# Kernel tuning notes

Measured on AMD Instinct MI355X. Metric: run time of the kernel, lower is better.

Reference implementation:

```python
import jax, jax.numpy as jnp
from jax import lax
import numpy as np

B, K, H, W = 16, 8, 256, 256


def setup_inputs() -> dict:
    key = jax.random.key(0)
    masks = jax.random.normal(key, (B, K, H, W), dtype=jnp.float32)
    return {"masks": masks}


def _nlccs_loss_one(mask):
    """Per-mask loss. mask: (H, W) float, already rescaled/clamped.

    Replicates cv2.connectedComponentsWithStats (8-connectivity, background is
    a single label regardless of connectivity), sorts components by area, and
    suppresses (zeroes a pmask over) the bounding box of the second-largest
    component, then returns mean(pmask * mask).
    """
    h, w = mask.shape
    S = h * w  # sentinel / background label
    sent = jnp.int32(S)
    fg = lax.stop_gradient(mask) > 0.5  # cv2 threshold (arr > 0.5)
    idx = jnp.arange(S, dtype=jnp.int32).reshape(h, w)
    lab0 = jnp.where(fg, idx, sent)

    def step(lab):
        # 8-connectivity neighbor-min propagation (cv2 default connectivity=8)
        p = jnp.pad(lab, 1, constant_values=S)
        m = lab
        for dy in (-1, 0, 1):
            for dx in (-1, 0, 1):
                if dy == 0 and dx == 0:
                    continue
                m = jnp.minimum(m, p[1 + dy:1 + dy + h, 1 + dx:1 + dx + w])
        lab = jnp.where(fg, m, sent)
        # pointer jumping: lab <- lab[lab] for log-time convergence
        ext = jnp.concatenate([lab.reshape(-1), jnp.array([S], jnp.int32)])
        return jnp.where(fg, ext[lab], sent)

    def cond(c):
        lab, prev = c
        return jnp.any(lab != prev)

    def body(c):
        lab, _ = c
        return step(lab), lab

    lab, _ = lax.while_loop(cond, body, (step(lab0), lab0))

    # per-label areas; background pixels all share label S (like cv2 label 0)
    areas = jnp.zeros(S + 1, jnp.int32).at[lab.reshape(-1)].add(1)
    _, top_idx = lax.top_k(areas, 2)
    second = top_idx[1]  # stats sorted by area -> stats[-2]

    # bounding box of the second-largest component
    sel = lab == second
    rows = jnp.arange(h, dtype=jnp.int32)[:, None]
    cols = jnp.arange(w, dtype=jnp.int32)[None, :]
    h0 = jnp.min(jnp.where(sel, rows, h))
    h1 = jnp.max(jnp.where(sel, rows, -1)) + 1
    w0 = jnp.min(jnp.where(sel, cols, w))
    w1 = jnp.max(jnp.where(sel, cols, -1)) + 1
    inside = (rows >= h0) & (rows < h1) & (cols >= w0) & (cols < w1)
    pmask = 1.0 - inside.astype(mask.dtype)  # pmask[h0:h1, w0:w1] = 0
    return (pmask * mask).mean()


def reference(masks):
    # masks: (b, k, h, w)
    m = jnp.maximum((masks + 1.0) * 0.5, 0.0)  # ((masks+1)/2).clamp(min=0)
    flat = m.reshape(-1, m.shape[-2], m.shape[-1])  # (b*k, h, w)
    losses = jax.vmap(_nlccs_loss_one)(flat)
    return losses.mean()
```

## Files before the change

kernel.cpp:

```cpp
#include <hip/hip_runtime.h>

#define HH 256
#define WW 256
#define SS 65536
#define NM 128
#define TRR 16
#define NT2 16
#define RMX 2048
#define SPT 1024
#define SPM 16384

struct Meta {
  double dsum[NM];
  int h0[NM]; int h1[NM]; int w0[NM]; int w1[NM];
};

__device__ __forceinline__ int find_c(int* L, int x) {
  int p = L[x];
  if (p == x) return x;
  int root = p, q = L[root];
  while (q != root) { root = q; q = L[root]; }
  if (root != p) L[x] = root;
  return root;
}

__device__ void unite(int* L, int a, int b) {
  bool done = false;
  do {
    a = find_c(L, a);
    b = find_c(L, b);
    if (a < b)      { int old = atomicMin(&L[b], a); done = (old == b); b = old; }
    else if (b < a) { int old = atomicMin(&L[a], b); done = (old == a); a = old; }
    else done = true;
  } while (!done);
}

__device__ __forceinline__ int find_halve(int* L, int x) {
  int p = L[x];
  while (p != x) {
    int gp = L[p];
    if (gp == p) return p;
    L[x] = gp;
    x = p; p = gp;
  }
  return x;
}

__device__ __forceinline__ int cid(const unsigned long long* rm,
                                   const int* rpre, int r) {
  int w = r >> 6, b = r & 63;
  return rpre[w] + (int)__popcll(rm[w] & (b ? ((1ull << b) - 1) : 0ull));
}

__device__ __forceinline__ unsigned long long mask_le(int b) {
  return (b == 63) ? ~0ull : ((1ull << (b + 1)) - 1);
}
__device__ __forceinline__ unsigned long long mask_lt(int b) {
  return b ? ((1ull << b) - 1) : 0ull;
}

__global__ __launch_bounds__(512)
void k_local(const float* __restrict__ in, int cb,
             int* __restrict__ gp, int* __restrict__ ga,
             unsigned int* __restrict__ gbb, unsigned short* __restrict__ gl,
             unsigned short* __restrict__ gbrow, int* __restrict__ gnr,
             double* __restrict__ tdsum, unsigned int* __restrict__ tbb,
             int* __restrict__ gfg0) {
  __shared__ unsigned long long sfgw[TRR][4];
  __shared__ unsigned char sfgc[TRR][32];
  __shared__ unsigned long long srs[TRR][4];
  __shared__ int wpre64[64];
  __shared__ int snr;
  __shared__ int sspan[RMX];
  __shared__ int suf[RMX];
  __shared__ unsigned long long rootm[32];
  __shared__ int rpre[32];
  __shared__ int sA[SPT], sW0[SPT], sW1[SPT], sH0[SPT], sH1[SPT];
  __shared__ double sred[8];
  __shared__ int sbb[4][8];

  int q = blockIdx.x, lm = q >> 4, tile = q & 15;
  int tid = threadIdx.x, lane = tid & 63, wv = tid >> 6;
  int gm = cb + lm, R0 = tile << 4;

  int r1 = tid >> 5, cs = tid & 31;
  const float4* src =
      (const float4*)(in + ((size_t)gm << 16) + ((R0 + r1) << 8) + (cs << 3));
  double dsum = 0.0;
  unsigned int fgb = 0;
  for (int k = 0; k < 2; k++) {
    float4 v = src[k];
    float m0 = fmaxf((v.x + 1.0f) * 0.5f, 0.0f);
    float m1 = fmaxf((v.y + 1.0f) * 0.5f, 0.0f);
    float m2 = fmaxf((v.z + 1.0f) * 0.5f, 0.0f);
    float m3 = fmaxf((v.w + 1.0f) * 0.5f, 0.0f);
    dsum += (double)m0 + (double)m1 + (double)m2 + (double)m3;
    fgb |= ((m0 > 0.5f) ? 1u : 0u) << (4 * k);
    fgb |= ((m1 > 0.5f) ? 1u : 0u) << (4 * k + 1);
    fgb |= ((m2 > 0.5f) ? 1u : 0u) << (4 * k + 2);
    fgb |= ((m3 > 0.5f) ? 1u : 0u) << (4 * k + 3);
  }
  sfgc[r1][cs] = (unsigned char)fgb;
  __syncthreads();
  if (tid < 64) {
    int row = tid >> 2, w = tid & 3;
    const unsigned char* pc = &sfgc[row][w << 3];
    unsigned long long wd = 0;
    for (int i = 0; i < 8; i++) wd |= ((unsigned long long)pc[i]) << (i << 3);
    sfgw[row][w] = wd;
  }
  __syncthreads();

  if (tid < 64) {
    int row = tid >> 2, w = tid & 3;
    unsigned long long W = sfgw[row][w];
    unsigned long long carry = (w > 0) ? (sfgw[row][w - 1] >> 63) : 0ull;
    unsigned long long rs = W & ~((W << 1) | carry);
    srs[row][w] = rs;
    int cnt = (int)__popcll(rs);
    int sa = cnt;
    for (int off = 1; off < 64; off <<= 1) {
      int t = __shfl_up(sa, off);
      if (tid >= off) sa += t;
    }
    wpre64[tid] = sa - cnt;
    if (tid == 63) snr = sa;
    int id = sa - cnt;
    unsigned long long bits = rs;
    while (bits) {
      int a = (int)__ffsll(bits) - 1;
      bits &= bits - 1;
      int A = (w << 6) + a;
      unsigned long long inv = ~(W >> a);
      int len = inv ? ((int)__ffsll(inv) - 1) : (64 - a);
      if (len == 64 - a) {
        for (int w2 = w + 1; w2 < 4; w2++) {
          unsigned long long iv2 = ~sfgw[row][w2];
          int t = iv2 ? ((int)__ffsll(iv2) - 1) : 64;
          len += t;
          if (t < 64) break;
        }
      }
      sspan[id] = (row << 16) | (A << 8) | (A + len - 1);
      suf[id] = id;
      id++;
    }
  } else {
    for (int s = tid - 64; s < SPT; s += 448) {
      sA[s] = 0; sW0[s] = WW; sW1[s] = -1; sH0[s] = TRR; sH1[s] = -1;
    }
  }
  __syncthreads();

  int nr = snr;

  for (int i = tid; i < nr; i += 512) {
    int sp = sspan[i];
    int row = sp >> 16, a = (sp >> 8) & 255, b = sp & 255;
    if (row == 0) continue;
    int lo = max(a - 1, 0), hi = min(b + 1, 255);
    const unsigned long long* Wp = sfgw[row - 1];
    const unsigned long long* Rp = srs[row - 1];
    int prebase = (row - 1) << 2;
    int lw = lo >> 6, lb = lo & 63;
    if (((Wp[lw] >> lb) & 1) && !((Rp[lw] >> lb) & 1)) {
      int j = wpre64[prebase + lw] + (int)__popcll(Rp[lw] & mask_le(lb)) - 1;
      unite(suf, i, j);
    }
    for (int w = lw; w <= (hi >> 6); w++) {
      unsigned long long m = Rp[w];
      if (w == lw) m &= ~mask_lt(lb);
      if (w == (hi >> 6)) m &= mask_le(hi & 63);
      int base2 = wpre64[prebase + w];
      while (m) {
        int bb = (int)__ffsll(m) - 1;
        m &= m - 1;
        int j = base2 + (int)__popcll(Rp[w] & mask_lt(bb));
        unite(suf, i, j);
      }
    }
  }
  __syncthreads();

  for (int j = 0; j < 4; j++) {
    int i = tid + (j << 9);
    unsigned long long bal = __ballot(i < nr && suf[i] == i);
    if (lane == 0) rootm[wv + (j << 3)] = bal;
  }
  __syncthreads();
  if (tid < 32) {
    int pc = (int)__popcll(rootm[tid]);
    int sa = pc;
    for (int off = 1; off < 32; off <<= 1) {
      int t = __shfl_up(sa, off);
      if (tid >= off) sa += t;
    }
    rpre[tid] = sa - pc;
  }
  __syncthreads();

  for (int i = tid; i < nr; i += 512) {
    int root = find_halve(suf, i);
    int id = cid(rootm, rpre, root);
    int sp = sspan[i];
    int row = sp >> 16, a = (sp >> 8) & 255, b = sp & 255;
    atomicAdd(&sA[id], b - a + 1);
    if (a < sW0[id]) atomicMin(&sW0[id], a);
    if (b > sW1[id]) atomicMax(&sW1[id], b);
    if (row < sH0[id]) atomicMin(&sH0[id], row);
    if (row > sH1[id]) atomicMax(&sH1[id], row);
  }
  __syncthreads();

  int nc = rpre[31] + (int)__popcll(rootm[31]);
  for (int i = tid; i < nr; i += 512) {
    if (suf[i] == i) {
      int id = cid(rootm, rpre, i);
      int gid = (lm << 14) + (tile << 10) + id;
      int sp = sspan[i];
      gp[gid] = gid;
      ga[gid] = sA[id];
      gl[gid] = (unsigned short)((tile << 12) + ((sp >> 16) << 8) +
                                 ((sp >> 8) & 255));
      gbb[gid] = ((unsigned)(R0 + sH0[id]) << 24) | ((unsigned)sW0[id] << 16)
               | ((unsigned)(R0 + sH1[id]) << 8) | (unsigned)sW1[id];
    }
  }
  {
    int c = tid & 255, topbot = tid >> 8;
    int brow = topbot ? (TRR - 1) : 0;
    unsigned short val = 0xFFFF;
    if ((sfgw[brow][c >> 6] >> (c & 63)) & 1) {
      int w = c >> 6, bb = c & 63;
      int id = wpre64[(brow << 2) + w] +
               (int)__popcll(srs[brow][w] & mask_le(bb)) - 1;
      int root = find_halve(suf, id);
      val = (unsigned short)((tile << 10) + cid(rootm, rpre, root));
    }
    gbrow[(q << 9) + (topbot ? 256 : 0) + c] = val;
  }
  if (tid == 0) gnr[q] = nc;

  int c = tid & 255, half = (tid >> 8) << 3;
  int bh0r = TRR, bh1r = -1;
  bool anybg = false;
  for (int row = half; row < half + 8; row++) {
    if (!((sfgw[row][c >> 6] >> (c & 63)) & 1)) {
      anybg = true;
      bh0r = min(bh0r, row); bh1r = max(bh1r, row);
    }
  }
  int bw0r = anybg ? c : WW, bw1r = anybg ? c : -1;
  for (int off = 32; off > 0; off >>= 1) {
    bw0r = min(bw0r, __shfl_down(bw0r, off));
    bw1r = max(bw1r, __shfl_down(bw1r, off));
    bh0r = min(bh0r, __shfl_down(bh0r, off));
    bh1r = max(bh1r, __shfl_down(bh1r, off));
  }
  if (lane == 0) { sbb[0][wv] = bw0r; sbb[1][wv] = bw1r;
                   sbb[2][wv] = bh0r; sbb[3][wv] = bh1r; }
  for (int off = 32; off > 0; off >>= 1) dsum += __shfl_down(dsum, off);
  if (lane == 0) sred[wv] = dsum;
  __syncthreads();
  if (tid == 0) {
    int a0 = sbb[0][0], a1 = sbb[1][0], a2 = sbb[2][0], a3 = sbb[3][0];
    for (int i = 1; i < 8; i++) {
      a0 = min(a0, sbb[0][i]); a1 = max(a1, sbb[1][i]);
      a2 = min(a2, sbb[2][i]); a3 = max(a3, sbb[3][i]);
    }
    unsigned pack = (a1 >= 0)
        ? (((unsigned)(R0 + a2) << 24) | ((unsigned)a0 << 16) |
           ((unsigned)(R0 + a3) << 8) | (unsigned)a1)
        : 0xFFFF0000u;
    tbb[q] = pack;
    double t = 0.0;
    for (int i = 0; i < 8; i++) t += sred[i];
    tdsum[q] = t;
    if (tile == 0) gfg0[lm] = (int)(sfgw[0][0] & 1ull);
  }
}

__global__ void k_seam(int* __restrict__ gp,
                       const unsigned short* __restrict__ gbrow) {
  int b = blockIdx.x;
  int lm = b / 15, s = b % 15;
  int tb = lm << 4;
  int sbase = lm << 14;
  const unsigned short* up = gbrow + ((tb + s) << 9) + 256;
  const unsigned short* lo = gbrow + ((tb + s + 1) << 9);
  int c = threadIdx.x;
  unsigned short v16 = lo[c];
  if (v16 == 0xFFFF) return;
  int v = sbase + v16;
  bool wfg = (c > 0) && (lo[c - 1] != 0xFFFF);
  unsigned short n16 = up[c];
  if (!wfg) {
    if (n16 != 0xFFFF) unite(gp, v, sbase + n16);
    else if (c > 0 && up[c - 1] != 0xFFFF) unite(gp, v, sbase + up[c - 1]);
  }
  if (n16 == 0xFFFF && c < 255 && up[c + 1] != 0xFFFF)
    unite(gp, v, sbase + up[c + 1]);
}

__global__ void k_push(int* __restrict__ gp, int* __restrict__ ga,
                       unsigned int* __restrict__ gbb,
                       const int* __restrict__ gnr) {
  int q = blockIdx.x;
  int lm = q >> 4;
  int sbase = lm << 14;
  int nc = gnr[q];
  int tid = threadIdx.x, lane = tid & 63;
  for (int t = 0; t < 4; t++) {
    int slot = (t << 8) + tid;
    int r = -1, a = 0;
    int h0 = HH, w0 = WW, h1 = -1, w1 = -1;
    if (slot < nc) {
      int gid = sbase + ((q & 15) << 10) + slot;
      int rr = find_c(gp, gid);
      if (rr != gid) {
        r = rr; a = ga[gid];
        unsigned int bb = gbb[gid];
        h0 = (int)(bb >> 24); w0 = (int)((bb >> 16) & 255);
        h1 = (int)((bb >> 8) & 255); w1 = (int)(bb & 255);
      }
    }
    bool pend = (r >= 0);
    while (__any(pend)) {
      unsigned long long mk = __ballot(pend);
      int srcl = (int)__ffsll(mk) - 1;
      int lead = __shfl(r, srcl);
      bool mine = pend && (r == lead);
      int v  = mine ? a  : 0;
      int g0 = mine ? h0 : HH;
      int g1 = mine ? h1 : -1;
      int g2 = mine ? w0 : WW;
      int g3 = mine ? w1 : -1;
      for (int off = 32; off > 0; off >>= 1) {
        v += __shfl_down(v, off);
        g0 = min(g0, __shfl_down(g0, off));
        g1 = max(g1, __shfl_down(g1, off));
        g2 = min(g2, __shfl_down(g2, off));
        g3 = max(g3, __shfl_down(g3, off));
      }
      int tot = __shfl(v, 0);
      int m0 = __shfl(g0, 0), m1 = __shfl(g1, 0);
      int m2 = __shfl(g2, 0), m3 = __shfl(g3, 0);
      if (lane == srcl) {
        atomicAdd(&ga[lead], tot);
        unsigned int* dst = &gbb[lead];
        unsigned int old = *dst;
        while (true) {
          int oh0 = (int)(old >> 24), ow0 = (int)((old >> 16) & 255);
          int oh1 = (int)((old >> 8) & 255), ow1 = (int)(old & 255);
          int nh0 = min(oh0, m0), nw0 = min(ow0, m2);
          int nh1 = max(oh1, m1), nw1 = max(ow1, m3);
          unsigned int mrg = ((unsigned)nh0 << 24) | ((unsigned)nw0 << 16) |
                             ((unsigned)nh1 << 8) | (unsigned)nw1;
          if (mrg == old) break;
          unsigned int got = atomicCAS(dst, old, mrg);
          if (got == old) break;
          old = got;
        }
      }
      pend = pend && !mine;
    }
  }
}

__global__ void k_top2p(const int* __restrict__ gp, const int* __restrict__ ga,
                        const unsigned short* __restrict__ gl,
                        const int* __restrict__ gnr,
                        unsigned long long* __restrict__ tt1,
                        unsigned long long* __restrict__ tt2,
                        int* __restrict__ tfs) {
  int q = blockIdx.x;
  int lm = q >> 4, tile = q & 15;
  int sbase = lm << 14;
  int nc = gnr[q];
  int tid = threadIdx.x, lane = tid & 63, wv = tid >> 6;
  unsigned long long t1 = 0, t2 = 0;
  int fsum = 0;
  for (int sl = tid; sl < nc; sl += 256) {
    int s = (tile << 10) + sl;
    int gid = sbase + s;
    if (gp[gid] == gid) {
      int a = ga[gid];
      int lab = gl[gid];
      fsum += a;
      unsigned long long key = ((unsigned long long)a << 37)
                             | ((unsigned long long)(SS - lab) << 20)
                             | (unsigned)s;
      if (key > t1) { t2 = t1; t1 = key; }
      else if (key > t2) t2 = key;
    }
  }
  for (int off = 32; off > 0; off >>= 1) {
    unsigned long long o1 = __shfl_down(t1, off), o2 = __shfl_down(t2, off);
    if (o1 > t1) { t2 = (t1 > o2) ? t1 : o2; t1 = o1; }
    else if (o1 > t2) t2 = o1;
    fsum += __shfl_down(fsum, off);
  }
  __shared__ unsigned long long s1[4], s2[4];
  __shared__ int sf[4];
  if (lane == 0) { s1[wv] = t1; s2[wv] = t2; sf[wv] = fsum; }
  __syncthreads();
  if (tid == 0) {
    for (int i = 1; i < 4; i++) {
      unsigned long long o1 = s1[i], o2 = s2[i];
      if (o1 > t1) { t2 = (t1 > o2) ? t1 : o2; t1 = o1; }
      else if (o1 > t2) t2 = o1;
      fsum += sf[i];
    }
    tt1[q] = t1; tt2[q] = t2; tfs[q] = fsum;
  }
}

__global__ __launch_bounds__(64)
void k_mask(const double* __restrict__ tdsum,
            const unsigned int* __restrict__ tbb,
            const unsigned long long* __restrict__ tt1,
            const unsigned long long* __restrict__ tt2,
            const int* __restrict__ tfs, const int* __restrict__ gfg0,
            const unsigned int* __restrict__ gbb,
            Meta* __restrict__ mt, int c0) {
  int lm = blockIdx.x, gm = c0 + lm;
  int tid = threadIdx.x;
  int tb = lm << 4;
  double d = 0.0;
  int h0 = 255, w0 = 255, h1 = 0, w1 = 0;
  unsigned long long t1 = 0, t2 = 0;
  int fsum = 0;
  if (tid < 16) {
    d = tdsum[tb + tid];
    unsigned bb = tbb[tb + tid];
    h0 = (int)(bb >> 24); w0 = (int)((bb >> 16) & 255);
    h1 = (int)((bb >> 8) & 255); w1 = (int)(bb & 255);
    t1 = tt1[tb + tid]; t2 = tt2[tb + tid]; fsum = tfs[tb + tid];
  }
  for (int off = 8; off > 0; off >>= 1) {
    d += __shfl_down(d, off);
    h0 = min(h0, __shfl_down(h0, off));
    w0 = min(w0, __shfl_down(w0, off));
    h1 = max(h1, __shfl_down(h1, off));
    w1 = max(w1, __shfl_down(w1, off));
    unsigned long long o1 = __shfl_down(t1, off), o2 = __shfl_down(t2, off);
    if (o1 > t1) { t2 = (t1 > o2) ? t1 : o2; t1 = o1; }
    else if (o1 > t2) t2 = o1;
    fsum += __shfl_down(fsum, off);
  }
  if (tid == 0) {
    mt->dsum[gm] = d;
    unsigned long long bg = ((unsigned long long)(SS - fsum)) << 37;
    int zl = gfg0[lm] ? 1 : 0;
    unsigned long long zk = ((unsigned long long)(SS - zl)) << 20;
    if (bg > t1) { t2 = t1; t1 = bg; } else if (bg > t2) t2 = bg;
    if (zk > t1) { t2 = t1; t1 = zk; } else if (zk > t2) t2 = zk;
    if (t2 == bg) {
      mt->h0[gm] = h0; mt->h1[gm] = h1; mt->w0[gm] = w0; mt->w1[gm] = w1;
    } else if (t2 == zk) {
      mt->h0[gm] = 1; mt->h1[gm] = 0; mt->w0[gm] = 1; mt->w1[gm] = 0;
    } else {
      unsigned int bb = gbb[(lm << 14) + (int)(t2 & 0xFFFFF)];
      mt->h0[gm] = (int)(bb >> 24);
      mt->w0[gm] = (int)((bb >> 16) & 255);
      mt->h1[gm] = (int)((bb >> 8) & 255);
      mt->w1[gm] = (int)(bb & 255);
    }
  }
}

__global__ void k_inside(const float* __restrict__ in,
                         const Meta* __restrict__ mt,
                         double* __restrict__ dinsp, int c0) {
  int b = blockIdx.x;
  int lm = b >> 3, seg = b & 7;
  int gm = c0 + lm;
  int h0 = mt->h0[gm], h1 = mt->h1[gm], w0 = mt->w0[gm], w1 = mt->w1[gm];
  double acc = 0.0;
  if (h1 >= h0) {
    int cc = w0 + threadIdx.x;
    if (cc <= w1) {
      const float* base = in + ((size_t)gm << 16);
      for (int rr = h0 + seg; rr <= h1; rr += 8) {
        float x = base[(rr << 8) + cc];
        acc += (double)fmaxf((x + 1.0f) * 0.5f, 0.0f);
      }
    }
  }
  for (int off = 32; off > 0; off >>= 1) acc += __shfl_down(acc, off);
  __shared__ double sd[4];
  int wid = threadIdx.x >> 6, lane = threadIdx.x & 63;
  if (lane == 0) sd[wid] = acc;
  __syncthreads();
  if (threadIdx.x == 0)
    dinsp[(gm << 3) + seg] = sd[0] + sd[1] + sd[2] + sd[3];
}

__global__ void k_final(const Meta* __restrict__ mt,
                        const double* __restrict__ dinsp,
                        float* __restrict__ out) {
  __shared__ double sd[NM];
  int t = threadIdx.x;
  double di = 0.0;
  for (int s = 0; s < 8; s++) di += dinsp[(t << 3) + s];
  sd[t] = (mt->dsum[t] - di) / (double)SS;
  __syncthreads();
  for (int off = 64; off > 0; off >>= 1) {
    if (t < off) sd[t] += sd[t + off];
    __syncthreads();
  }
  if (t == 0) out[0] = (float)(sd[0] / (double)NM);
}

extern "C" void kernel_launch(void* const* d_in, const int* in_sizes, int n_in,
                              void* d_out, int out_size, void* d_ws,
                              size_t ws_size, hipStream_t stream) {
  const float* in = (const float*)d_in[0];
  float* out = (float*)d_out;

  Meta* mt = (Meta*)d_ws;
  const size_t meta_bytes = (sizeof(Meta) + 255) & ~(size_t)255;
  char* base = (char*)d_ws + meta_bytes;
  size_t fixed = (size_t)NM * 8 * sizeof(double);
  size_t avail = (ws_size > meta_bytes + fixed)
                     ? (ws_size - meta_bytes - fixed) : 0;
  const size_t per_mask = (size_t)NT2 * 8 + NT2 * 4 + 4 +
                          (size_t)SPM * (4 + 4 + 4 + 2) +
                          (size_t)NT2 * 512 * 2 + NT2 * 4 +
                          (size_t)NT2 * (8 + 8 + 4);
  int chunk = (int)(avail / per_mask);
  if (chunk > NM) chunk = NM;
  if (chunk < 1) return;

  char* ptr = base;
  double* dinsp = (double*)ptr;        ptr += fixed;
  double* tdsum = (double*)ptr;        ptr += (size_t)chunk * NT2 * 8;
  unsigned long long* tt1 = (unsigned long long*)ptr;
  ptr += (size_t)chunk * NT2 * 8;
  unsigned long long* tt2 = (unsigned long long*)ptr;
  ptr += (size_t)chunk * NT2 * 8;
  int* gp = (int*)ptr;                 ptr += (size_t)chunk * SPM * 4;
  int* ga = (int*)ptr;                 ptr += (size_t)chunk * SPM * 4;
  unsigned int* gbb = (unsigned int*)ptr;       ptr += (size_t)chunk * SPM * 4;
  unsigned short* gl = (unsigned short*)ptr;    ptr += (size_t)chunk * SPM * 2;
  unsigned short* gbrow = (unsigned short*)ptr; ptr += (size_t)chunk * NT2 * 512 * 2;
  int* gnr = (int*)ptr;                ptr += (size_t)chunk * NT2 * 4;
  unsigned int* tbb = (unsigned int*)ptr;       ptr += (size_t)chunk * NT2 * 4;
  int* tfs = (int*)ptr;                ptr += (size_t)chunk * NT2 * 4;
  int* gfg0 = (int*)ptr;

  for (int c0 = 0; c0 < NM; c0 += chunk) {
    int cn = (chunk < NM - c0) ? chunk : (NM - c0);
    k_local<<<cn * NT2, 512, 0, stream>>>(in, c0, gp, ga, gbb, gl, gbrow,
                                          gnr, tdsum, tbb, gfg0);
    k_seam <<<cn * 15, 256, 0, stream>>>(gp, gbrow);
    k_push <<<cn * NT2, 256, 0, stream>>>(gp, ga, gbb, gnr);
    k_top2p<<<cn * NT2, 256, 0, stream>>>(gp, ga, gl, gnr, tt1, tt2, tfs);
    k_mask <<<cn, 64, 0, stream>>>(tdsum, tbb, tt1, tt2, tfs, gfg0, gbb,
                                   mt, c0);
    k_inside<<<cn * 8, 256, 0, stream>>>(in, mt, dinsp, c0);
  }
  k_final<<<1, 128, 0, stream>>>(mt, dinsp, out);
}
```

Before: 184.6 us.

## Fold seam, mask and final kernels into predecessors via last-block counters

Removes three separate kernel launches per chunk (seam union, per-mask metadata, final reduction) by appending their work to the preceding kernels. Each preceding kernel's last-finishing block does the extra work, found with an atomic counter plus threadfence. The counters are zeroed by one memset each call. This cuts launch and inter-kernel gaps, at the cost of serialising the seam unions inside a single block per mask and adding atomic and fence overhead.

```diff
diff --git a/kernel.cpp b/kernel.cpp
--- a/kernel.cpp
+++ b/kernel.cpp
@@ -65,7 +65,7 @@
              unsigned int* __restrict__ gbb, unsigned short* __restrict__ gl,
              unsigned short* __restrict__ gbrow, int* __restrict__ gnr,
              double* __restrict__ tdsum, unsigned int* __restrict__ tbb,
-             int* __restrict__ gfg0) {
+             int* __restrict__ gfg0, int* __restrict__ cntA) {
   __shared__ unsigned long long sfgw[TRR][4];
   __shared__ unsigned char sfgc[TRR][32];
   __shared__ unsigned long long srs[TRR][4];
@@ -78,6 +78,7 @@
   __shared__ int sA[SPT], sW0[SPT], sW1[SPT], sH0[SPT], sH1[SPT];
   __shared__ double sred[8];
   __shared__ int sbb[4][8];
+  __shared__ int slast;
 
   int q = blockIdx.x, lm = q >> 4, tile = q & 15;
   int tid = threadIdx.x, lane = tid & 63, wv = tid >> 6;
@@ -278,28 +279,32 @@
     tdsum[q] = t;
     if (tile == 0) gfg0[lm] = (int)(sfgw[0][0] & 1ull);
   }
-}
-
-__global__ void k_seam(int* __restrict__ gp,
-                       const unsigned short* __restrict__ gbrow) {
-  int b = blockIdx.x;
-  int lm = b / 15, s = b % 15;
-  int tb = lm << 4;
-  int sbase = lm << 14;
-  const unsigned short* up = gbrow + ((tb + s) << 9) + 256;
-  const unsigned short* lo = gbrow + ((tb + s + 1) << 9);
-  int c = threadIdx.x;
-  unsigned short v16 = lo[c];
-  if (v16 == 0xFFFF) return;
-  int v = sbase + v16;
-  bool wfg = (c > 0) && (lo[c - 1] != 0xFFFF);
-  unsigned short n16 = up[c];
-  if (!wfg) {
-    if (n16 != 0xFFFF) unite(gp, v, sbase + n16);
-    else if (c > 0 && up[c - 1] != 0xFFFF) unite(gp, v, sbase + up[c - 1]);
-  }
-  if (n16 == 0xFFFF && c < 255 && up[c + 1] != 0xFFFF)
-    unite(gp, v, sbase + up[c + 1]);
+
+  __threadfence();
+  __syncthreads();
+  if (tid == 0) slast = (atomicAdd(&cntA[gm], 1) == 15) ? 1 : 0;
+  __syncthreads();
+  if (slast) {
+    __threadfence();
+    int sbase = lm << 14;
+    for (int idx = tid; idx < 15 * 256; idx += 512) {
+      int s = idx >> 8, c2 = idx & 255;
+      const unsigned short* up = gbrow + (((lm << 4) + s) << 9) + 256;
+      const unsigned short* lo = gbrow + (((lm << 4) + s + 1) << 9);
+      unsigned short v16 = lo[c2];
+      if (v16 == 0xFFFF) continue;
+      int v = sbase + v16;
+      bool wfg = (c2 > 0) && (lo[c2 - 1] != 0xFFFF);
+      unsigned short n16 = up[c2];
+      if (!wfg) {
+        if (n16 != 0xFFFF) unite(gp, v, sbase + n16);
+        else if (c2 > 0 && up[c2 - 1] != 0xFFFF)
+          unite(gp, v, sbase + up[c2 - 1]);
+      }
+      if (n16 == 0xFFFF && c2 < 255 && up[c2 + 1] != 0xFFFF)
+        unite(gp, v, sbase + up[c2 + 1]);
+    }
+  }
 }
 
 __global__ void k_push(int* __restrict__ gp, int* __restrict__ ga,
@@ -372,12 +377,20 @@
                         const int* __restrict__ gnr,
                         unsigned long long* __restrict__ tt1,
                         unsigned long long* __restrict__ tt2,
-                        int* __restrict__ tfs) {
+                        int* __restrict__ tfs,
+                        const double* __restrict__ tdsum,
+                        const unsigned int* __restrict__ tbb,
+                        const int* __restrict__ gfg0,
+                        const unsigned int* __restrict__ gbb,
+                        int* __restrict__ cntB,
+                        Meta* __restrict__ mt, int c0) {
   int q = blockIdx.x;
   int lm = q >> 4, tile = q & 15;
+  int gm = c0 + lm;
   int sbase = lm << 14;
   int nc = gnr[q];
   int tid = threadIdx.x, lane = tid & 63, wv = tid >> 6;
+  __shared__ int slast;
   unsigned long long t1 = 0, t2 = 0;
   int fsum = 0;
   for (int sl = tid; sl < nc; sl += 256) {
@@ -413,65 +426,63 @@
     }
     tt1[q] = t1; tt2[q] = t2; tfs[q] = fsum;
   }
-}
-
-__global__ __launch_bounds__(64)
-void k_mask(const double* __restrict__ tdsum,
-            const unsigned int* __restrict__ tbb,
-            const unsigned long long* __restrict__ tt1,
-            const unsigned long long* __restrict__ tt2,
-            const int* __restrict__ tfs, const int* __restrict__ gfg0,
-            const unsigned int* __restrict__ gbb,
-            Meta* __restrict__ mt, int c0) {
-  int lm = blockIdx.x, gm = c0 + lm;
-  int tid = threadIdx.x;
-  int tb = lm << 4;
-  double d = 0.0;
-  int h0 = 255, w0 = 255, h1 = 0, w1 = 0;
-  unsigned long long t1 = 0, t2 = 0;
-  int fsum = 0;
-  if (tid < 16) {
-    d = tdsum[tb + tid];
-    unsigned bb = tbb[tb + tid];
-    h0 = (int)(bb >> 24); w0 = (int)((bb >> 16) & 255);
-    h1 = (int)((bb >> 8) & 255); w1 = (int)(bb & 255);
-    t1 = tt1[tb + tid]; t2 = tt2[tb + tid]; fsum = tfs[tb + tid];
-  }
-  for (int off = 8; off > 0; off >>= 1) {
-    d += __shfl_down(d, off);
-    h0 = min(h0, __shfl_down(h0, off));
-    w0 = min(w0, __shfl_down(w0, off));
-    h1 = max(h1, __shfl_down(h1, off));
-    w1 = max(w1, __shfl_down(w1, off));
-    unsigned long long o1 = __shfl_down(t1, off), o2 = __shfl_down(t2, off);
-    if (o1 > t1) { t2 = (t1 > o2) ? t1 : o2; t1 = o1; }
-    else if (o1 > t2) t2 = o1;
-    fsum += __shfl_down(fsum, off);
-  }
-  if (tid == 0) {
-    mt->dsum[gm] = d;
-    unsigned long long bg = ((unsigned long long)(SS - fsum)) << 37;
-    int zl = gfg0[lm] ? 1 : 0;
-    unsigned long long zk = ((unsigned long long)(SS - zl)) << 20;
-    if (bg > t1) { t2 = t1; t1 = bg; } else if (bg > t2) t2 = bg;
-    if (zk > t1) { t2 = t1; t1 = zk; } else if (zk > t2) t2 = zk;
-    if (t2 == bg) {
-      mt->h0[gm] = h0; mt->h1[gm] = h1; mt->w0[gm] = w0; mt->w1[gm] = w1;
-    } else if (t2 == zk) {
-      mt->h0[gm] = 1; mt->h1[gm] = 0; mt->w0[gm] = 1; mt->w1[gm] = 0;
-    } else {
-      unsigned int bb = gbb[(lm << 14) + (int)(t2 & 0xFFFFF)];
-      mt->h0[gm] = (int)(bb >> 24);
-      mt->w0[gm] = (int)((bb >> 16) & 255);
-      mt->h1[gm] = (int)((bb >> 8) & 255);
-      mt->w1[gm] = (int)(bb & 255);
+
+  __threadfence();
+  __syncthreads();
+  if (tid == 0) slast = (atomicAdd(&cntB[gm], 1) == 15) ? 1 : 0;
+  __syncthreads();
+  if (slast && wv == 0) {
+    __threadfence();
+    int tb = lm << 4;
+    double d = 0.0;
+    int h0 = 255, w0 = 255, h1 = 0, w1 = 0;
+    unsigned long long u1 = 0, u2 = 0;
+    int fs = 0;
+    if (lane < 16) {
+      d = tdsum[tb + lane];
+      unsigned bb = tbb[tb + lane];
+      h0 = (int)(bb >> 24); w0 = (int)((bb >> 16) & 255);
+      h1 = (int)((bb >> 8) & 255); w1 = (int)(bb & 255);
+      u1 = tt1[tb + lane]; u2 = tt2[tb + lane]; fs = tfs[tb + lane];
+    }
+    for (int off = 8; off > 0; off >>= 1) {
+      d += __shfl_down(d, off);
+      h0 = min(h0, __shfl_down(h0, off));
+      w0 = min(w0, __shfl_down(w0, off));
+      h1 = max(h1, __shfl_down(h1, off));
+      w1 = max(w1, __shfl_down(w1, off));
+      unsigned long long o1 = __shfl_down(u1, off), o2 = __shfl_down(u2, off);
+      if (o1 > u1) { u2 = (u1 > o2) ? u1 : o2; u1 = o1; }
+      else if (o1 > u2) u2 = o1;
+      fs += __shfl_down(fs, off);
+    }
+    if (lane == 0) {
+      mt->dsum[gm] = d;
+      unsigned long long bg = ((unsigned long long)(SS - fs)) << 37;
+      int zl = gfg0[lm] ? 1 : 0;
+      unsigned long long zk = ((unsigned long long)(SS - zl)) << 20;
+      if (bg > u1) { u2 = u1; u1 = bg; } else if (bg > u2) u2 = bg;
+      if (zk > u1) { u2 = u1; u1 = zk; } else if (zk > u2) u2 = zk;
+      if (u2 == bg) {
+        mt->h0[gm] = h0; mt->h1[gm] = h1; mt->w0[gm] = w0; mt->w1[gm] = w1;
+      } else if (u2 == zk) {
+        mt->h0[gm] = 1; mt->h1[gm] = 0; mt->w0[gm] = 1; mt->w1[gm] = 0;
+      } else {
+        unsigned int bb = gbb[(lm << 14) + (int)(u2 & 0xFFFFF)];
+        mt->h0[gm] = (int)(bb >> 24);
+        mt->w0[gm] = (int)((bb >> 16) & 255);
+        mt->h1[gm] = (int)((bb >> 8) & 255);
+        mt->w1[gm] = (int)(bb & 255);
+      }
     }
   }
 }
 
 __global__ void k_inside(const float* __restrict__ in,
                          const Meta* __restrict__ mt,
-                         double* __restrict__ dinsp, int c0) {
+                         double* __restrict__ dinsp, int c0,
+                         int* __restrict__ cntC, int nb, int do_final,
+                         float* __restrict__ out) {
   int b = blockIdx.x;
   int lm = b >> 3, seg = b & 7;
   int gm = c0 + lm;
@@ -494,22 +505,31 @@
   __syncthreads();
   if (threadIdx.x == 0)
     dinsp[(gm << 3) + seg] = sd[0] + sd[1] + sd[2] + sd[3];
-}
-
-__global__ void k_final(const Meta* __restrict__ mt,
-                        const double* __restrict__ dinsp,
-                        float* __restrict__ out) {
-  __shared__ double sd[NM];
-  int t = threadIdx.x;
-  double di = 0.0;
-  for (int s = 0; s < 8; s++) di += dinsp[(t << 3) + s];
-  sd[t] = (mt->dsum[t] - di) / (double)SS;
-  __syncthreads();
-  for (int off = 64; off > 0; off >>= 1) {
-    if (t < off) sd[t] += sd[t + off];
+
+  if (do_final) {
+    __shared__ int sflag;
+    if (threadIdx.x == 0) {
+      __threadfence();
+      sflag = (atomicAdd(cntC, 1) == nb - 1) ? 1 : 0;
+    }
     __syncthreads();
-  }
-  if (t == 0) out[0] = (float)(sd[0] / (double)NM);
+    if (sflag) {
+      __threadfence();
+      __shared__ double sd2[NM];
+      int t = threadIdx.x;
+      if (t < NM) {
+        double di = 0.0;
+        for (int s = 0; s < 8; s++) di += dinsp[(t << 3) + s];
+        sd2[t] = (mt->dsum[t] - di) / (double)SS;
+      }
+      __syncthreads();
+      for (int off = 64; off > 0; off >>= 1) {
+        if (t < off) sd2[t] += sd2[t + off];
+        __syncthreads();
+      }
+      if (t == 0) out[0] = (float)(sd2[0] / (double)NM);
+    }
+  }
 }
 
 extern "C" void kernel_launch(void* const* d_in, const int* in_sizes, int n_in,
@@ -521,7 +541,8 @@
   Meta* mt = (Meta*)d_ws;
   const size_t meta_bytes = (sizeof(Meta) + 255) & ~(size_t)255;
   char* base = (char*)d_ws + meta_bytes;
-  size_t fixed = (size_t)NM * 8 * sizeof(double);
+  const size_t cnt_bytes = ((size_t)(NM * 2 + 1) * 4 + 255) & ~(size_t)255;
+  size_t fixed = (size_t)NM * 8 * sizeof(double) + cnt_bytes;
   size_t avail = (ws_size > meta_bytes + fixed)
                      ? (ws_size - meta_bytes - fixed) : 0;
   const size_t per_mask = (size_t)NT2 * 8 + NT2 * 4 + 4 +
@@ -533,7 +554,11 @@
   if (chunk < 1) return;
 
   char* ptr = base;
-  double* dinsp = (double*)ptr;        ptr += fixed;
+  double* dinsp = (double*)ptr;        ptr += (size_t)NM * 8 * 8;
+  int* cntA = (int*)ptr;
+  int* cntB = cntA + NM;
+  int* cntC = cntB + NM;
+  ptr += cnt_bytes;
   double* tdsum = (double*)ptr;        ptr += (size_t)chunk * NT2 * 8;
   unsigned long long* tt1 = (unsigned long long*)ptr;
   ptr += (size_t)chunk * NT2 * 8;
@@ -549,16 +574,18 @@
   int* tfs = (int*)ptr;                ptr += (size_t)chunk * NT2 * 4;
   int* gfg0 = (int*)ptr;
 
+  hipMemsetAsync(cntA, 0, (size_t)(NM * 2 + 1) * 4, stream);
+
   for (int c0 = 0; c0 < NM; c0 += chunk) {
     int cn = (chunk < NM - c0) ? chunk : (NM - c0);
+    int do_final = (c0 + cn >= NM) ? 1 : 0;
     k_local<<<cn * NT2, 512, 0, stream>>>(in, c0, gp, ga, gbb, gl, gbrow,
-                                          gnr, tdsum, tbb, gfg0);
-    k_seam <<<cn * 15, 256, 0, stream>>>(gp, gbrow);
+                                          gnr, tdsum, tbb, gfg0, cntA);
     k_push <<<cn * NT2, 256, 0, stream>>>(gp, ga, gbb, gnr);
-    k_top2p<<<cn * NT2, 256, 0, stream>>>(gp, ga, gl, gnr, tt1, tt2, tfs);
-    k_mask <<<cn, 64, 0, stream>>>(tdsum, tbb, tt1, tt2, tfs, gfg0, gbb,
-                                   mt, c0);
-    k_inside<<<cn * 8, 256, 0, stream>>>(in, mt, dinsp, c0);
-  }
-  k_final<<<1, 128, 0, stream>>>(mt, dinsp, out);
-}
+    k_top2p<<<cn * NT2, 256, 0, stream>>>(gp, ga, gl, gnr, tt1, tt2, tfs,
+                                          tdsum, tbb, gfg0, gbb, cntB, mt,
+                                          c0);
+    k_inside<<<cn * 8, 256, 0, stream>>>(in, mt, dinsp, c0, cntC, cn * 8,
+                                         do_final, out);
+  }
+}
```

Result: slower. 714.3 us (+287.0%).
